# Performance work log

Measured on AMD Instinct MI355X. Metric: run time of the kernel, lower is better.

## Reference

```python
import jax, jax.numpy as jnp
import numpy as np

K = 3   # kernel_size
D = 1   # dilation
G = 8   # groups
BN_EPS = 1e-5


def setup_inputs() -> dict:
    key = jax.random.key(0)
    ks = jax.random.split(key, 8)
    N, C, H, W = 8, 64, 256, 256
    k2 = K * K
    x = jax.random.normal(ks[0], (N, C, H, W), jnp.float32)
    conv_w = jax.random.normal(ks[1], (G * k2, C), jnp.float32) * (2.0 / C) ** 0.5
    bn_gamma = jnp.ones((G * k2,), jnp.float32)
    bn_beta = jnp.zeros((G * k2,), jnp.float32)
    bn_mean = jax.random.normal(ks[2], (G * k2,), jnp.float32) * 0.01
    bn_var = jax.random.uniform(ks[3], (G * k2,), jnp.float32, 0.5, 1.5)
    lamb_l = jax.random.normal(ks[4], (C,), jnp.float32) * 0.1
    lamb_h = jax.random.normal(ks[5], (C,), jnp.float32) * 0.1
    inside_all = jax.random.normal(ks[6], (C, 1, 1), jnp.float32) * 0.1
    return {"x": x, "conv_w": conv_w, "bn_gamma": bn_gamma, "bn_beta": bn_beta,
            "bn_mean": bn_mean, "bn_var": bn_var, "lamb_l": lamb_l,
            "lamb_h": lamb_h, "inside_all": inside_all}


def reference(x, conv_w, bn_gamma, bn_beta, bn_mean, bn_var, lamb_l, lamb_h, inside_all):
    N, C, H, W = x.shape
    k2 = K * K
    # ap: adaptive avg pool to (1,1) -> (N, C)
    pooled = x.mean(axis=(2, 3))
    # 1x1 conv on a 1x1 map == matmul; then eval-mode BatchNorm
    lf = pooled @ conv_w.T                                   # (N, G*k2)
    lf = (lf - bn_mean) * (bn_gamma / jnp.sqrt(bn_var + BN_EPS)) + bn_beta
    lf = jnp.tanh(lf).reshape(N, G, 1, k2, 1)                # (N, G, 1, k2, 1)
    # im2col/unfold with reflection padding; ordering matches torch (C, kh, kw)
    p = D * (K - 1) // 2
    xp = jnp.pad(x, ((0, 0), (0, 0), (p, p), (p, p)), mode="reflect")
    patches = jnp.stack(
        [xp[:, :, i * D:i * D + H, j * D:j * D + W] for i in range(K) for j in range(K)],
        axis=2,
    )                                                        # (N, C, k2, H, W)
    xu = patches.reshape(N, G, C // G, k2, H * W)
    low_part = jnp.sum(xu * lf, axis=3).reshape(N, C, H, W)  # per-pixel dynamic filter
    # DSA: gap pools to (1,1)
    gap = x.mean(axis=(2, 3), keepdims=True)                 # (N, C, 1, 1)
    out_low = (low_part * (inside_all + 1.0) - inside_all * gap) * lamb_l[None, :, None, None]
    out_high = x * (lamb_h[None, :, None, None] + 1.0)
    return out_low + out_high
```

## Files before the change

### kernel.cpp

```cpp
#include <hip/hip_runtime.h>
#include <math.h>

#define NN 8
#define CC 64
#define HH 256
#define WW 256
#define GG 8
#define K2 9
#define OC 72
#define BN_EPS 1e-5f

__global__ __launch_bounds__(1024) void pool_kernel(const float* __restrict__ x,
                                                    float* __restrict__ pooled) {
    int nc = blockIdx.x;
    const float4* p4 = (const float4*)(x + (size_t)nc * (HH * WW));
    float s = 0.f;
#pragma unroll 4
    for (int i = threadIdx.x; i < (HH * WW) / 4; i += 1024) {
        float4 v = p4[i];
        s += (v.x + v.y) + (v.z + v.w);
    }
    for (int off = 32; off > 0; off >>= 1) s += __shfl_down(s, off, 64);
    __shared__ float smem[16];
    int lane = threadIdx.x & 63, wid = threadIdx.x >> 6;
    if (lane == 0) smem[wid] = s;
    __syncthreads();
    if (threadIdx.x < 16) {
        float t = smem[threadIdx.x];
        for (int off = 8; off > 0; off >>= 1) t += __shfl_down(t, off, 64);
        if (threadIdx.x == 0) pooled[nc] = t * (1.0f / (HH * WW));
    }
}

__global__ __launch_bounds__(256) void lf_kernel(const float* __restrict__ pooled,
                                                 const float* __restrict__ conv_w,
                                                 const float* __restrict__ gamma,
                                                 const float* __restrict__ beta,
                                                 const float* __restrict__ mean,
                                                 const float* __restrict__ var,
                                                 float* __restrict__ lf) {
    int j = blockIdx.x * blockDim.x + threadIdx.x;
    if (j >= NN * OC) return;
    int n = j / OC, oc = j % OC;
    const float* pw = conv_w + oc * CC;
    const float* pp = pooled + n * CC;
    float acc = 0.f;
#pragma unroll 8
    for (int c = 0; c < CC; ++c) acc += pp[c] * pw[c];
    float inv = gamma[oc] / sqrtf(var[oc] + BN_EPS);
    lf[j] = tanhf((acc - mean[oc]) * inv + beta[oc]);
}

__global__ __launch_bounds__(256) void main_kernel(const float* __restrict__ x,
                                                   const float* __restrict__ lf,
                                                   const float* __restrict__ pooled,
                                                   const float* __restrict__ lamb_l,
                                                   const float* __restrict__ lamb_h,
                                                   const float* __restrict__ ia,
                                                   float* __restrict__ out) {
    const int wid  = threadIdx.x >> 6;
    const int lane = threadIdx.x & 63;
    const int nc   = blockIdx.x >> 4;
    const int r0   = ((blockIdx.x & 15) << 4) + (wid << 2);
    const int c    = nc & (CC - 1);
    const int n    = nc >> 6;
    const int g    = c >> 3;

    const float* lw = lf + (n * OC + g * K2);
    const float w00 = lw[0], w01 = lw[1], w02 = lw[2];
    const float w10 = lw[3], w11 = lw[4], w12 = lw[5];
    const float w20 = lw[6], w21 = lw[7], w22 = lw[8];
    const float ll    = lamb_l[c];
    const float lh1   = lamb_h[c] + 1.0f;
    const float iav   = ia[c];
    const float scale = iav + 1.0f;
    const float bias  = -iav * pooled[nc];

    const float* base = x + (size_t)nc * (HH * WW);

    float4 v[6];
    float  L[6], R[6];
#pragma unroll
    for (int i = 0; i < 6; ++i) {
        int r = r0 - 1 + i;
        r = (r < 0) ? 1 : ((r > HH - 1) ? HH - 2 : r);
        v[i] = ((const float4*)(base + r * WW))[lane];
    }
#pragma unroll
    for (int i = 0; i < 6; ++i) {
        L[i] = __shfl_up(v[i].w, 1, 64);   if (lane == 0)  L[i] = v[i].y;
        R[i] = __shfl_down(v[i].x, 1, 64); if (lane == 63) R[i] = v[i].z;
    }

    float* outbase = out + (size_t)nc * (HH * WW);
#pragma unroll
    for (int j = 0; j < 4; ++j) {
        const float t[6] = {L[j],   v[j].x,   v[j].y,   v[j].z,   v[j].w,   R[j]};
        const float m[6] = {L[j+1], v[j+1].x, v[j+1].y, v[j+1].z, v[j+1].w, R[j+1]};
        const float b[6] = {L[j+2], v[j+2].x, v[j+2].y, v[j+2].z, v[j+2].w, R[j+2]};
        float4 o;
        float* op = &o.x;
#pragma unroll
        for (int k = 0; k < 4; ++k) {
            float acc = w00 * t[k] + w01 * t[k + 1] + w02 * t[k + 2]
                      + w10 * m[k] + w11 * m[k + 1] + w12 * m[k + 2]
                      + w20 * b[k] + w21 * b[k + 1] + w22 * b[k + 2];
            op[k] = ll * (scale * acc + bias) + lh1 * m[k + 1];
        }
        ((float4*)(outbase + (size_t)(r0 + j) * WW))[lane] = o;
    }
}

extern "C" void kernel_launch(void* const* d_in, const int* in_sizes, int n_in,
                              void* d_out, int out_size, void* d_ws, size_t ws_size,
                              hipStream_t stream) {
    const float* x      = (const float*)d_in[0];
    const float* conv_w = (const float*)d_in[1];
    const float* gamma  = (const float*)d_in[2];
    const float* beta   = (const float*)d_in[3];
    const float* mean   = (const float*)d_in[4];
    const float* var    = (const float*)d_in[5];
    const float* lamb_l = (const float*)d_in[6];
    const float* lamb_h = (const float*)d_in[7];
    const float* ia     = (const float*)d_in[8];
    float* out = (float*)d_out;

    float* pooled = (float*)d_ws;
    float* lf     = pooled + NN * CC;

    pool_kernel<<<NN * CC, 1024, 0, stream>>>(x, pooled);
    lf_kernel<<<(NN * OC + 255) / 256, 256, 0, stream>>>(pooled, conv_w, gamma, beta,
                                                         mean, var, lf);
    main_kernel<<<NN * CC * (HH / 16), 256, 0, stream>>>(x, lf, pooled, lamb_l, lamb_h,
                                                         ia, out);
}
```

Measured before the change: 266.5 us.

## Fuse lf computation into main kernel, enlarge row tile, use nontemporal stores

Removes the separate lf kernel launch by having each wavefront recompute its group's nine dynamic filter weights via a wave-wide dot-product reduction over channels. Each wave now processes 8 output rows instead of 4, which cuts the halo reload ratio and halves the grid size. Output stores become nontemporal so they don't pollute cache. The cost is redundant per-wave conv/tanh work and higher register pressure from the larger tile.

```diff
diff --git a/kernel.cpp b/kernel.cpp
--- a/kernel.cpp
+++ b/kernel.cpp
@@ -9,6 +9,8 @@
 #define K2 9
 #define OC 72
 #define BN_EPS 1e-5f
+
+typedef float vfloat4 __attribute__((ext_vector_type(4)));
 
 __global__ __launch_bounds__(1024) void pool_kernel(const float* __restrict__ x,
                                                     float* __restrict__ pooled) {
@@ -32,44 +34,40 @@
     }
 }
 
-__global__ __launch_bounds__(256) void lf_kernel(const float* __restrict__ pooled,
-                                                 const float* __restrict__ conv_w,
-                                                 const float* __restrict__ gamma,
-                                                 const float* __restrict__ beta,
-                                                 const float* __restrict__ mean,
-                                                 const float* __restrict__ var,
-                                                 float* __restrict__ lf) {
-    int j = blockIdx.x * blockDim.x + threadIdx.x;
-    if (j >= NN * OC) return;
-    int n = j / OC, oc = j % OC;
-    const float* pw = conv_w + oc * CC;
-    const float* pp = pooled + n * CC;
-    float acc = 0.f;
-#pragma unroll 8
-    for (int c = 0; c < CC; ++c) acc += pp[c] * pw[c];
-    float inv = gamma[oc] / sqrtf(var[oc] + BN_EPS);
-    lf[j] = tanhf((acc - mean[oc]) * inv + beta[oc]);
-}
-
 __global__ __launch_bounds__(256) void main_kernel(const float* __restrict__ x,
-                                                   const float* __restrict__ lf,
                                                    const float* __restrict__ pooled,
+                                                   const float* __restrict__ conv_w,
+                                                   const float* __restrict__ gamma,
+                                                   const float* __restrict__ beta,
+                                                   const float* __restrict__ mean,
+                                                   const float* __restrict__ var,
                                                    const float* __restrict__ lamb_l,
                                                    const float* __restrict__ lamb_h,
                                                    const float* __restrict__ ia,
                                                    float* __restrict__ out) {
     const int wid  = threadIdx.x >> 6;
     const int lane = threadIdx.x & 63;
-    const int nc   = blockIdx.x >> 4;
-    const int r0   = ((blockIdx.x & 15) << 4) + (wid << 2);
+    const int nc   = blockIdx.x >> 3;
+    const int r0   = ((blockIdx.x & 7) << 5) + (wid << 3);
     const int c    = nc & (CC - 1);
     const int n    = nc >> 6;
     const int g    = c >> 3;
 
-    const float* lw = lf + (n * OC + g * K2);
-    const float w00 = lw[0], w01 = lw[1], w02 = lw[2];
-    const float w10 = lw[3], w11 = lw[4], w12 = lw[5];
-    const float w20 = lw[6], w21 = lw[7], w22 = lw[8];
+    const float pc = pooled[n * CC + lane];
+    float wgt[K2];
+#pragma unroll
+    for (int q = 0; q < K2; ++q) {
+        const int oc = g * K2 + q;
+        float part = pc * conv_w[oc * CC + lane];
+        for (int off = 32; off > 0; off >>= 1) part += __shfl_down(part, off, 64);
+        const float dot = __shfl(part, 0, 64);
+        const float inv = gamma[oc] * rsqrtf(var[oc] + BN_EPS);
+        wgt[q] = tanhf((dot - mean[oc]) * inv + beta[oc]);
+    }
+    const float w00 = wgt[0], w01 = wgt[1], w02 = wgt[2];
+    const float w10 = wgt[3], w11 = wgt[4], w12 = wgt[5];
+    const float w20 = wgt[6], w21 = wgt[7], w22 = wgt[8];
+
     const float ll    = lamb_l[c];
     const float lh1   = lamb_h[c] + 1.0f;
     const float iav   = ia[c];
@@ -78,36 +76,35 @@
 
     const float* base = x + (size_t)nc * (HH * WW);
 
-    float4 v[6];
-    float  L[6], R[6];
+    float4 v[10];
+    float  L[10], R[10];
 #pragma unroll
-    for (int i = 0; i < 6; ++i) {
+    for (int i = 0; i < 10; ++i) {
         int r = r0 - 1 + i;
         r = (r < 0) ? 1 : ((r > HH - 1) ? HH - 2 : r);
         v[i] = ((const float4*)(base + r * WW))[lane];
     }
 #pragma unroll
-    for (int i = 0; i < 6; ++i) {
+    for (int i = 0; i < 10; ++i) {
         L[i] = __shfl_up(v[i].w, 1, 64);   if (lane == 0)  L[i] = v[i].y;
         R[i] = __shfl_down(v[i].x, 1, 64); if (lane == 63) R[i] = v[i].z;
     }
 
     float* outbase = out + (size_t)nc * (HH * WW);
 #pragma unroll
-    for (int j = 0; j < 4; ++j) {
+    for (int j = 0; j < 8; ++j) {
         const float t[6] = {L[j],   v[j].x,   v[j].y,   v[j].z,   v[j].w,   R[j]};
         const float m[6] = {L[j+1], v[j+1].x, v[j+1].y, v[j+1].z, v[j+1].w, R[j+1]};
         const float b[6] = {L[j+2], v[j+2].x, v[j+2].y, v[j+2].z, v[j+2].w, R[j+2]};
-        float4 o;
-        float* op = &o.x;
+        vfloat4 o;
 #pragma unroll
         for (int k = 0; k < 4; ++k) {
             float acc = w00 * t[k] + w01 * t[k + 1] + w02 * t[k + 2]
                       + w10 * m[k] + w11 * m[k + 1] + w12 * m[k + 2]
                       + w20 * b[k] + w21 * b[k + 1] + w22 * b[k + 2];
-            op[k] = ll * (scale * acc + bias) + lh1 * m[k + 1];
+            o[k] = ll * (scale * acc + bias) + lh1 * m[k + 1];
         }
-        ((float4*)(outbase + (size_t)(r0 + j) * WW))[lane] = o;
+        __builtin_nontemporal_store(o, (vfloat4*)(outbase + (size_t)(r0 + j) * WW) + lane);
     }
 }
 
@@ -126,11 +123,8 @@
     float* out = (float*)d_out;
 
     float* pooled = (float*)d_ws;
-    float* lf     = pooled + NN * CC;
 
     pool_kernel<<<NN * CC, 1024, 0, stream>>>(x, pooled);
-    lf_kernel<<<(NN * OC + 255) / 256, 256, 0, stream>>>(pooled, conv_w, gamma, beta,
-                                                         mean, var, lf);
-    main_kernel<<<NN * CC * (HH / 16), 256, 0, stream>>>(x, lf, pooled, lamb_l, lamb_h,
-                                                         ia, out);
+    main_kernel<<<NN * CC * (HH / 32), 256, 0, stream>>>(x, pooled, conv_w, gamma, beta,
+                                                         mean, var, lamb_l, lamb_h, ia, out);
 }
```

Measured after the change: 270.7 us. No clear change (+1.6%).
